# Performance work log

Measured on AMD Instinct MI355X. Metric: run time of the kernel, lower is better.

Reference implementation:

```python
import jax, jax.numpy as jnp
import numpy as np

START_IDX = 1  # undefined global `start_idx` in the source; fixed BOS id


def _lstm_gates(x_t, h, c, Wih, Whh, b):
    # PyTorch LSTM gate order: i, f, g, o
    gates = x_t @ Wih.T + h @ Whh.T + b
    i, f, g, o = jnp.split(gates, 4, axis=-1)
    c_new = jax.nn.sigmoid(f) * c + jax.nn.sigmoid(i) * jnp.tanh(g)
    h_new = jax.nn.sigmoid(o) * jnp.tanh(c_new)
    return h_new, c_new


def setup_inputs() -> dict:
    key = jax.random.key(0)
    ks = jax.random.split(key, 14)
    B, T, H, Vin, Vout = 64, 64, 512, 32000, 32000
    Hh = H // 2
    f = lambda k, shp, s=0.1: (jax.random.normal(k, shp) * s).astype(jnp.float32)
    return {
        "x": jax.random.randint(ks[0], (B, T), 0, Vin),
        "enc_emb": f(ks[1], (Vin, H), 0.2),
        "enc_wih_f": f(ks[2], (4 * Hh, H)),
        "enc_whh_f": f(ks[3], (4 * Hh, Hh)),
        "enc_b_f": jnp.zeros((4 * Hh,), jnp.float32),
        "enc_wih_b": f(ks[4], (4 * Hh, H)),
        "enc_whh_b": f(ks[5], (4 * Hh, Hh)),
        "enc_b_b": jnp.zeros((4 * Hh,), jnp.float32),
        "dec_emb": f(ks[6], (Vout, H), 0.2),
        "dec_wih": f(ks[7], (4 * H, H)),
        "dec_whh": f(ks[8], (4 * H, H)),
        "dec_b": jnp.zeros((4 * H,), jnp.float32),
        "clf_w": f(ks[9], (Vout, H), 0.2),
        "clf_b": jnp.zeros((Vout,), jnp.float32),
    }


def reference(x, enc_emb, enc_wih_f, enc_whh_f, enc_b_f,
              enc_wih_b, enc_whh_b, enc_b_b,
              dec_emb, dec_wih, dec_whh, dec_b, clf_w, clf_b):
    B, T = x.shape
    H = enc_emb.shape[1]
    Hh = H // 2

    # ---- Encoder: 1-layer bidirectional LSTM, hidden Hh per direction ----
    emb = enc_emb[x]                       # [B, T, H]
    xs = emb.transpose(1, 0, 2)            # [T, B, H] (scan over time)

    def run_dir(seq, Wih, Whh, b):
        def step(carry, xt):
            h, c = carry
            h, c = _lstm_gates(xt, h, c, Wih, Whh, b)
            return (h, c), None
        h0 = jnp.zeros((B, Hh), emb.dtype)
        (h, c), _ = jax.lax.scan(step, (h0, h0), seq)
        return h, c

    hf, cf = run_dir(xs, enc_wih_f, enc_whh_f, enc_b_f)
    hb, cb = run_dir(xs[::-1], enc_wih_b, enc_whh_b, enc_b_b)
    # hidden reshape in _forward_encoder: concat fwd/bwd final states -> [B, H]
    dec_h = jnp.concatenate([hf, hb], axis=-1)
    dec_c = jnp.concatenate([cf, cb], axis=-1)

    # ---- Decoder: greedy self-feeding loop for T-1 steps ----
    def dec_step(carry, _):
        h, c, y = carry
        e = dec_emb[y]                                  # [B, H]
        h, c = _lstm_gates(e, h, c, dec_wih, dec_whh, dec_b)
        logits = h @ clf_w.T + clf_b                    # [B, Vout]
        # argmax(softmax(logits)) == argmax(logits)
        y = jnp.argmax(logits, axis=-1)
        return (h, c, y), logits

    y0 = jnp.full((B,), START_IDX, dtype=x.dtype)
    _, logits = jax.lax.scan(dec_step, (dec_h, dec_c, y0), None, length=T - 1)
    # torch.cat(H, dim=2) with h.unsqueeze(2): [B, Vout, T-1]
    return logits.transpose(1, 2, 0)
```

## Files before the change

kernel.cpp:

```cpp
#include <hip/hip_runtime.h>
#include <math.h>

#define AM_PLAIN 0
#define AM_ENC   1
#define CM_PLAIN 0

typedef short bf16x8 __attribute__((ext_vector_type(8)));
typedef float f32x4 __attribute__((ext_vector_type(4)));

__device__ __forceinline__ float sigf(float x) { return 1.0f / (1.0f + expf(-x)); }

__device__ __forceinline__ unsigned short bf_rne(float f) {
  unsigned u = __float_as_uint(f);
  u += 0x7FFFu + ((u >> 16) & 1u);
  return (unsigned short)(u >> 16);
}
__device__ __forceinline__ float bf_f(unsigned short h) {
  return __uint_as_float(((unsigned)h) << 16);
}

template<int AMODE, int BTWO, int CMODE, int CDIR>
__global__ __launch_bounds__(256)
void gemm_k(const float* __restrict__ Ap, int lda,
            const float* __restrict__ emb,
            const int* __restrict__ xidx,
            const float* __restrict__ hbuf,
            const unsigned long long* __restrict__ cand_in, int nblk_cand, int step,
            const float* __restrict__ B0, const float* __restrict__ B1, int ldb,
            const float* __restrict__ bias,
            float* __restrict__ Cp, int ldc, long long zstride, int kper,
            unsigned long long* __restrict__ cand_out,
            float* __restrict__ dout, int tcol)
{
  __shared__ float As[32][68];
  __shared__ float Bs[32][68];
  __shared__ int ys[(AMODE == AM_PLAIN) ? 1 : 64];

  const int tid = threadIdx.x;
  const int tx = tid & 15, my = tid >> 4;
  const int n0 = tx * 4, m0 = my * 4;
  const int nbase = blockIdx.x * 64, mbase = blockIdx.y * 64;
  const int bz = blockIdx.z;

  if (AMODE == AM_ENC) {
    if (tid < 64) ys[tid] = xidx[tid * 64 + blockIdx.y];
  }
  if (AMODE != AM_PLAIN) __syncthreads();

  float acc[4][4];
#pragma unroll
  for (int i = 0; i < 4; ++i)
#pragma unroll
    for (int j = 0; j < 4; ++j) acc[i][j] = 0.0f;

  const int kbeg = bz * kper;
  const int lrow = tid >> 3, lk = (tid & 7) * 4;

  for (int kc = 0; kc < kper; kc += 32) {
    const int kg = kbeg + kc;
#pragma unroll
    for (int rr = 0; rr < 64; rr += 32) {
      const int row = lrow + rr;
      const float* ap;
      if (AMODE == AM_PLAIN) {
        ap = Ap + (size_t)(mbase + row) * lda + kg + lk;
      } else {
        ap = emb + (size_t)ys[row] * 512 + kg + lk;
      }
      const float4 v = *(const float4*)ap;
      As[lk + 0][row] = v.x; As[lk + 1][row] = v.y;
      As[lk + 2][row] = v.z; As[lk + 3][row] = v.w;

      const int n = nbase + row;
      const float* bp = B0 + (size_t)n * ldb + kg + lk;
      const float4 w = *(const float4*)bp;
      Bs[lk + 0][row] = w.x; Bs[lk + 1][row] = w.y;
      Bs[lk + 2][row] = w.z; Bs[lk + 3][row] = w.w;
    }
    __syncthreads();
#pragma unroll
    for (int k = 0; k < 32; ++k) {
      const float4 a = *(const float4*)&As[k][m0];
      const float4 b = *(const float4*)&Bs[k][n0];
      acc[0][0] += a.x * b.x; acc[0][1] += a.x * b.y; acc[0][2] += a.x * b.z; acc[0][3] += a.x * b.w;
      acc[1][0] += a.y * b.x; acc[1][1] += a.y * b.y; acc[1][2] += a.y * b.z; acc[1][3] += a.y * b.w;
      acc[2][0] += a.z * b.x; acc[2][1] += a.z * b.y; acc[2][2] += a.z * b.z; acc[2][3] += a.z * b.w;
      acc[3][0] += a.w * b.x; acc[3][1] += a.w * b.y; acc[3][2] += a.w * b.z; acc[3][3] += a.w * b.w;
    }
    __syncthreads();
  }

#pragma unroll
  for (int i = 0; i < 4; ++i) {
    const int m = mbase + m0 + i;
#pragma unroll
    for (int j = 0; j < 4; ++j) {
      const int n = nbase + n0 + j;
      float v = acc[i][j];
      if (bias) v += bias[n];
      Cp[bz * zstride + (size_t)m * ldc + n] = v;
    }
  }
}

__global__ __launch_bounds__(1024)
void enc_mstep(const float* __restrict__ xwf, const float* __restrict__ xwb,
               const short* __restrict__ whhfF, const short* __restrict__ whhfB,
               const short* __restrict__ hin, short* __restrict__ hout,
               float* __restrict__ cbuf, float* __restrict__ hfinal, int s)
{
  __shared__ float gl[2][4][64][16];

  const int blk = blockIdx.x;
  const int d = blk >> 4;
  const int jb = blk & 15;
  const int j0 = jb * 16;
  const float* xw = d ? xwb : xwf;
  const short* wf = d ? whhfB : whhfF;
  const short* hi_ = hin + d * 32768;
  short* ho_ = hout + d * 32768;
  const int t = d ? (63 - s) : s;

  const int tid = threadIdx.x;
  const int lane = tid & 63, wv = tid >> 6;
  const int g = wv & 3, mh = (wv >> 2) & 1, kh = wv >> 3;
  const int lrow = lane & 15, lq = lane >> 4;
  const int ntile = g * 16 + jb;

  f32x4 acc[2];
#pragma unroll
  for (int mtl = 0; mtl < 2; ++mtl) acc[mtl] = (f32x4){0.f, 0.f, 0.f, 0.f};

#pragma unroll
  for (int kk = 0; kk < 4; ++kk) {
    const int kc = kh * 4 + kk;
    const short* wb = wf + ((size_t)(ntile * 8 + kc)) * 1024 + lane * 8;
    const bf16x8 bhi = *(const bf16x8*)wb;
    const bf16x8 blo = *(const bf16x8*)(wb + 512);
#pragma unroll
    for (int mtl = 0; mtl < 2; ++mtl) {
      const int mt = mh * 2 + mtl;
      const short* ab = hi_ + ((size_t)(mt * 8 + kc)) * 1024 + lane * 8;
      const bf16x8 ahi = *(const bf16x8*)ab;
      const bf16x8 alo = *(const bf16x8*)(ab + 512);
      acc[mtl] = __builtin_amdgcn_mfma_f32_16x16x32_bf16(ahi, bhi, acc[mtl], 0, 0, 0);
      acc[mtl] = __builtin_amdgcn_mfma_f32_16x16x32_bf16(alo, bhi, acc[mtl], 0, 0, 0);
      acc[mtl] = __builtin_amdgcn_mfma_f32_16x16x32_bf16(ahi, blo, acc[mtl], 0, 0, 0);
    }
  }

#pragma unroll
  for (int mtl = 0; mtl < 2; ++mtl)
#pragma unroll
    for (int r = 0; r < 4; ++r) {
      const int b = (mh * 2 + mtl) * 16 + lq * 4 + r;
      gl[kh][g][b][lrow] = acc[mtl][r];
    }
  __syncthreads();

  {
    const int b = tid >> 4, jl = tid & 15;
    const int j = j0 + jl;
    const float* xrow = xw + ((size_t)(t * 64 + b)) * 1024;
    const float gi = gl[0][0][b][jl] + gl[1][0][b][jl] + xrow[0 * 256 + j];
    const float gf = gl[0][1][b][jl] + gl[1][1][b][jl] + xrow[1 * 256 + j];
    const float gg = gl[0][2][b][jl] + gl[1][2][b][jl] + xrow[2 * 256 + j];
    const float go = gl[0][3][b][jl] + gl[1][3][b][jl] + xrow[3 * 256 + j];
    const size_t off = (size_t)b * 512 + d * 256 + j;
    const float cn = sigf(gf) * cbuf[off] + sigf(gi) * tanhf(gg);
    cbuf[off] = cn;
    const float hn = sigf(go) * tanhf(cn);
    const unsigned short hh = bf_rne(hn);
    const unsigned short ll = bf_rne(hn - bf_f(hh));
    const int mt = b >> 4;
    const int base = ((mt * 8 + (j >> 5)) * 2) * 512 + (((j >> 3) & 3) * 16 + (b & 15)) * 8 + (j & 7);
    ho_[base] = (short)hh;
    ho_[base + 512] = (short)ll;
    if (s == 63) hfinal[off] = hn;
  }
}

__global__ void kinit2(float* __restrict__ c, int* __restrict__ he)
{
  const int i = blockIdx.x * 256 + threadIdx.x;
  if (i < 32768) { c[i] = 0.f; he[i] = 0; }
}

__global__ __launch_bounds__(256)
void wconv(const float* __restrict__ p0, const float* __restrict__ p1,
           int ld, int split, int KC, short* __restrict__ frag, int total)
{
  const int i = blockIdx.x * 256 + threadIdx.x;
  if (i >= total) return;
  const int lane = i & 63;
  const int ck = i >> 6;
  const int kc = ck % KC;
  const int nt = ck / KC;
  const int n = nt * 16 + (lane & 15);
  const int k0 = kc * 32 + (lane >> 4) * 8;
  const float* src = (k0 < split) ? (p0 + (size_t)n * ld + k0)
                                  : (p1 + (size_t)n * ld + (k0 - split));
  const float4 v0 = *(const float4*)src;
  const float4 v1 = *(const float4*)(src + 4);
  const float x[8] = {v0.x, v0.y, v0.z, v0.w, v1.x, v1.y, v1.z, v1.w};
  bf16x8 vh, vl;
#pragma unroll
  for (int e = 0; e < 8; ++e) {
    const unsigned short h = bf_rne(x[e]);
    vh[e] = (short)h;
    vl[e] = (short)bf_rne(x[e] - bf_f(h));
  }
  const size_t base = (size_t)ck * 1024 + lane * 8;
  *(bf16x8*)(frag + base) = vh;
  *(bf16x8*)(frag + base + 512) = vl;
}

__global__ __launch_bounds__(256)
void h2frag(const float* __restrict__ h, short* __restrict__ frag)
{
  const int i = blockIdx.x * 256 + threadIdx.x;
  const int lane = i & 63;
  const int ck = i >> 6;
  const int b = (ck >> 4) * 16 + (lane & 15);
  const int k0 = (ck & 15) * 32 + (lane >> 4) * 8;
  const float* src = h + (size_t)b * 512 + k0;
  const float4 v0 = *(const float4*)src;
  const float4 v1 = *(const float4*)(src + 4);
  const float x[8] = {v0.x, v0.y, v0.z, v0.w, v1.x, v1.y, v1.z, v1.w};
  bf16x8 vh, vl;
#pragma unroll
  for (int e = 0; e < 8; ++e) {
    const unsigned short hh = bf_rne(x[e]);
    vh[e] = (short)hh;
    vl[e] = (short)bf_rne(x[e] - bf_f(hh));
  }
  const size_t base = (size_t)ck * 1024 + lane * 8;
  *(bf16x8*)(frag + base) = vh;
  *(bf16x8*)(frag + base + 512) = vl;
}

__global__ __launch_bounds__(256)
void demb2bf(const float* __restrict__ demb, short* __restrict__ debf)
{
  const int i = blockIdx.x * 256 + threadIdx.x;
  if (i >= 2048000) return;
  const int r = i >> 6;
  const int k0 = (i & 63) * 8;
  const float* src = demb + (size_t)r * 512 + k0;
  const float4 v0 = *(const float4*)src;
  const float4 v1 = *(const float4*)(src + 4);
  const float x[8] = {v0.x, v0.y, v0.z, v0.w, v1.x, v1.y, v1.z, v1.w};
  bf16x8 vh, vl;
#pragma unroll
  for (int e = 0; e < 8; ++e) {
    const unsigned short h = bf_rne(x[e]);
    vh[e] = (short)h;
    vl[e] = (short)bf_rne(x[e] - bf_f(h));
  }
  *(bf16x8*)(debf + (size_t)r * 1024 + k0) = vh;
  *(bf16x8*)(debf + (size_t)r * 1024 + 512 + k0) = vl;
}

#define NBLK_CLF 500

__global__ __launch_bounds__(1024)
void dec_gates(const short* __restrict__ debf,
               const short* __restrict__ gfrag,
               const unsigned long long* __restrict__ cand, int step,
               const float* __restrict__ db,
               const short* __restrict__ hfin, short* __restrict__ hfout,
               float* __restrict__ cbuf)
{
  __shared__ int ys[64];
  __shared__ unsigned long long red[16 * 64];
  __shared__ float gl[2][4][64][16];

  const int tid = threadIdx.x;
  const int lane = tid & 63, wv = tid >> 6;
  const int g = wv & 3, mh = (wv >> 2) & 1, kh = wv >> 3;
  const int j0 = blockIdx.x * 16;
  const int ntile = g * 32 + blockIdx.x;
  const int lrow = lane & 15, lq = lane >> 4;

  if (step == 0) {
    if (tid < 64) ys[tid] = 1;
  } else {
    const int b = tid & 63, slot = tid >> 6;
    unsigned long long mv = 0;
    for (int i2 = slot; i2 < NBLK_CLF; i2 += 16) {
      const unsigned long long v = cand[(size_t)i2 * 64 + b];
      mv = v > mv ? v : mv;
    }
    red[slot * 64 + b] = mv;
    __syncthreads();
    if (tid < 64) {
      unsigned long long m = red[tid];
#pragma unroll
      for (int s2 = 1; s2 < 16; ++s2) {
        const unsigned long long v = red[s2 * 64 + tid];
        m = v > m ? v : m;
      }
      ys[tid] = (int)(0xFFFFFFFFu - (unsigned)(m & 0xFFFFFFFFull));
    }
  }
  __syncthreads();

  f32x4 acc[2];
#pragma unroll
  for (int mtl = 0; mtl < 2; ++mtl) acc[mtl] = (f32x4){0.f, 0.f, 0.f, 0.f};

  if (kh == 0) {
    for (int kc = 0; kc < 16; ++kc) {
      const short* wb = gfrag + ((size_t)(ntile * 32 + kc)) * 1024 + lane * 8;
      const bf16x8 bhi = *(const bf16x8*)wb;
      const bf16x8 blo = *(const bf16x8*)(wb + 512);
      const int k0 = kc * 32 + lq * 8;
#pragma unroll
      for (int mtl = 0; mtl < 2; ++mtl) {
        const int b = (mh * 2 + mtl) * 16 + lrow;
        const short* ap = debf + (size_t)ys[b] * 1024 + k0;
        const bf16x8 ahi = *(const bf16x8*)ap;
        const bf16x8 alo = *(const bf16x8*)(ap + 512);
        acc[mtl] = __builtin_amdgcn_mfma_f32_16x16x32_bf16(ahi, bhi, acc[mtl], 0, 0, 0);
        acc[mtl] = __builtin_amdgcn_mfma_f32_16x16x32_bf16(alo, bhi, acc[mtl], 0, 0, 0);
        acc[mtl] = __builtin_amdgcn_mfma_f32_16x16x32_bf16(ahi, blo, acc[mtl], 0, 0, 0);
      }
    }
  } else {
    for (int kc = 16; kc < 32; ++kc) {
      const short* wb = gfrag + ((size_t)(ntile * 32 + kc)) * 1024 + lane * 8;
      const bf16x8 bhi = *(const bf16x8*)wb;
      const bf16x8 blo = *(const bf16x8*)(wb + 512);
#pragma unroll
      for (int mtl = 0; mtl < 2; ++mtl) {
        const int mt = mh * 2 + mtl;
        const short* ab = hfin + ((size_t)(mt * 16 + (kc - 16))) * 1024 + lane * 8;
        const bf16x8 ahi = *(const bf16x8*)ab;
        const bf16x8 alo = *(const bf16x8*)(ab + 512);
        acc[mtl] = __builtin_amdgcn_mfma_f32_16x16x32_bf16(ahi, bhi, acc[mtl], 0, 0, 0);
        acc[mtl] = __builtin_amdgcn_mfma_f32_16x16x32_bf16(alo, bhi, acc[mtl], 0, 0, 0);
        acc[mtl] = __builtin_amdgcn_mfma_f32_16x16x32_bf16(ahi, blo, acc[mtl], 0, 0, 0);
      }
    }
  }

#pragma unroll
  for (int mtl = 0; mtl < 2; ++mtl)
#pragma unroll
    for (int r = 0; r < 4; ++r) {
      const int b = (mh * 2 + mtl) * 16 + lq * 4 + r;
      gl[kh][g][b][lrow] = acc[mtl][r];
    }
  __syncthreads();

  {
    const int b = tid >> 4, jl = tid & 15;
    const int j = j0 + jl;
    const float gi = gl[0][0][b][jl] + gl[1][0][b][jl] + db[j];
    const float gf = gl[0][1][b][jl] + gl[1][1][b][jl] + db[512 + j];
    const float gg = gl[0][2][b][jl] + gl[1][2][b][jl] + db[1024 + j];
    const float go = gl[0][3][b][jl] + gl[1][3][b][jl] + db[1536 + j];
    const size_t off = (size_t)b * 512 + j;
    const float cn = sigf(gf) * cbuf[off] + sigf(gi) * tanhf(gg);
    cbuf[off] = cn;
    const float hn = sigf(go) * tanhf(cn);
    const unsigned short hh = bf_rne(hn);
    const unsigned short hl2 = bf_rne(hn - bf_f(hh));
    const int mt = b >> 4;
    const int kc = j >> 5;
    const size_t base = ((size_t)(mt * 16 + kc)) * 1024 + ((((j & 31) >> 3) * 16) + (b & 15)) * 8 + (j & 7);
    hfout[base] = (short)hh;
    hfout[base + 512] = (short)hl2;
  }
}

template<int DIRECT>
__global__ __launch_bounds__(256)
void dec_clf(const short* __restrict__ hfrag, const short* __restrict__ wfrag,
             const float* __restrict__ clfb,
             float* __restrict__ dst, int tcol,
             unsigned long long* __restrict__ cand_out)
{
  __shared__ unsigned long long cl[4][64];
  const int tid = threadIdx.x;
  const int lane = tid & 63, wv = tid >> 6;
  const int ntile = blockIdx.x * 4 + wv;
  const int lrow = lane & 15, lq = lane >> 4;

  f32x4 acc[4];
#pragma unroll
  for (int mt = 0; mt < 4; ++mt) acc[mt] = (f32x4){0.f, 0.f, 0.f, 0.f};

#pragma unroll 2
  for (int kc = 0; kc < 16; ++kc) {
    const short* wb = wfrag + ((size_t)(ntile * 16 + kc)) * 1024 + lane * 8;
    const bf16x8 bhi = *(const bf16x8*)wb;
    const bf16x8 blo = *(const bf16x8*)(wb + 512);
#pragma unroll
    for (int mt = 0; mt < 4; ++mt) {
      const short* ab = hfrag + ((size_t)(mt * 16 + kc)) * 1024 + lane * 8;
      const bf16x8 ahi = *(const bf16x8*)ab;
      const bf16x8 alo = *(const bf16x8*)(ab + 512);
      acc[mt] = __builtin_amdgcn_mfma_f32_16x16x32_bf16(ahi, bhi, acc[mt], 0, 0, 0);
      acc[mt] = __builtin_amdgcn_mfma_f32_16x16x32_bf16(alo, bhi, acc[mt], 0, 0, 0);
      acc[mt] = __builtin_amdgcn_mfma_f32_16x16x32_bf16(ahi, blo, acc[mt], 0, 0, 0);
    }
  }

  const int v = ntile * 16 + lrow;
  const float bias = clfb[v];
#pragma unroll
  for (int mt = 0; mt < 4; ++mt) {
#pragma unroll
    for (int r = 0; r < 4; ++r) {
      const float val = acc[mt][r] + bias;
      const int b = mt * 16 + lq * 4 + r;
      if (DIRECT) __builtin_nontemporal_store(val, dst + ((size_t)b * 32000 + v) * 63 + tcol);
      else        __builtin_nontemporal_store(val, dst + (size_t)b * 32000 + v);
      unsigned u = __float_as_uint(val);
      u ^= (u & 0x80000000u) ? 0xFFFFFFFFu : 0x80000000u;
      unsigned long long p = ((unsigned long long)u << 32) |
                             (unsigned long long)(0xFFFFFFFFu - (unsigned)v);
#pragma unroll
      for (int m2 = 1; m2 < 16; m2 <<= 1) {
        const unsigned long long o = __shfl_xor(p, m2);
        p = o > p ? o : p;
      }
      if (lrow == 0) cl[wv][b] = p;
    }
  }
  __syncthreads();
  if (tid < 64) {
    unsigned long long m = cl[0][tid];
    const unsigned long long v1 = cl[1][tid];
    const unsigned long long v2 = cl[2][tid];
    const unsigned long long v3 = cl[3][tid];
    m = v1 > m ? v1 : m; m = v2 > m ? v2 : m; m = v3 > m ? v3 : m;
    cand_out[(size_t)blockIdx.x * 64 + tid] = m;
  }
}

__global__ __launch_bounds__(256)
void transpose_out(const float* __restrict__ ls, float* __restrict__ out)
{
  __shared__ float tile[128 * 63];
  const int b = blockIdx.y;
  const int v0 = blockIdx.x * 128;
  for (int idx = threadIdx.x; idx < 128 * 63; idx += 256) {
    const int t = idx >> 7, v = idx & 127;
    tile[v * 63 + t] = ls[((size_t)t * 64 + b) * 32000 + v0 + v];
  }
  __syncthreads();
  float4* o4 = (float4*)(out + ((size_t)b * 32000 + v0) * 63);
  const float4* t4 = (const float4*)tile;
  for (int i = threadIdx.x; i < (128 * 63) / 4; i += 256) o4[i] = t4[i];
}

extern "C" void kernel_launch(void* const* d_in, const int* in_sizes, int n_in,
                              void* d_out, int out_size, void* d_ws, size_t ws_size,
                              hipStream_t stream)
{
  const int*   x       = (const int*)d_in[0];
  const float* enc_emb = (const float*)d_in[1];
  const float* ewih_f  = (const float*)d_in[2];
  const float* ewhh_f  = (const float*)d_in[3];
  const float* eb_f    = (const float*)d_in[4];
  const float* ewih_b  = (const float*)d_in[5];
  const float* ewhh_b  = (const float*)d_in[6];
  const float* eb_b    = (const float*)d_in[7];
  const float* demb    = (const float*)d_in[8];
  const float* dwih    = (const float*)d_in[9];
  const float* dwhh    = (const float*)d_in[10];
  const float* db      = (const float*)d_in[11];
  const float* clfw    = (const float*)d_in[12];
  const float* clfb    = (const float*)d_in[13];
  float* out = (float*)d_out;
  float* ws  = (float*)d_ws;

  float* xwf = ws;
  float* xwb = xwf + 4194304;
  float* h0  = xwb + 4194304;
  float* h1  = h0 + 32768;
  float* cbf = h1 + 32768;
  unsigned long long* cand = (unsigned long long*)(cbf + 32768);
  short* wfrag  = (short*)(cbf + 32768 + 64000);
  short* gfrag  = wfrag + 32768000;
  short* hfragA = gfrag + 4194304;
  short* hfragB = hfragA + 65536;
  short* debf   = hfragB + 65536;
  short* ehfF   = debf + 32768000;
  short* ehfB   = ehfF + 524288;
  short* he0    = ehfB + 524288;
  short* he1    = he0 + 65536;
  float* ls = (float*)(he1 + 65536);
  const size_t need_f = 4194304ull * 2 + 32768ull * 3 + 64000ull
                      + 16384000ull + 2097152ull + 32768ull * 2
                      + 16384000ull + 262144ull * 2 + 32768ull * 2 + 129024000ull;
  const bool wspath = ws_size >= need_f * sizeof(float);

  kinit2<<<dim3(128), dim3(256), 0, stream>>>(cbf, (int*)he0);

  wconv<<<dim3(128), dim3(256), 0, stream>>>(ewhh_f, ewhh_f, 256, 256, 8, ehfF, 32768);
  wconv<<<dim3(128), dim3(256), 0, stream>>>(ewhh_b, ewhh_b, 256, 256, 8, ehfB, 32768);
  wconv<<<dim3(8000), dim3(256), 0, stream>>>(clfw, clfw, 512, 512, 16, wfrag, 2048000);
  wconv<<<dim3(1024), dim3(256), 0, stream>>>(dwih, dwhh, 512, 512, 32, gfrag, 262144);
  demb2bf<<<dim3(8000), dim3(256), 0, stream>>>(demb, debf);

  dim3 gx(16, 64, 1);
  gemm_k<AM_ENC, 0, CM_PLAIN, 0><<<gx, 256, 0, stream>>>(
      nullptr, 0, enc_emb, x, nullptr, nullptr, 0, 0,
      ewih_f, nullptr, 512, eb_f, xwf, 1024, 0, 512, nullptr, nullptr, 0);
  gemm_k<AM_ENC, 0, CM_PLAIN, 0><<<gx, 256, 0, stream>>>(
      nullptr, 0, enc_emb, x, nullptr, nullptr, 0, 0,
      ewih_b, nullptr, 512, eb_b, xwb, 1024, 0, 512, nullptr, nullptr, 0);

  for (int s = 0; s < 64; ++s) {
    const short* hin = (s & 1) ? he1 : he0;
    short* hout      = (s & 1) ? he0 : he1;
    enc_mstep<<<dim3(32), dim3(1024), 0, stream>>>(
        xwf, xwb, ehfF, ehfB, hin, hout, cbf, h0, s);
  }

  h2frag<<<dim3(16), dim3(256), 0, stream>>>(h0, hfragA);

  for (int t = 0; t < 63; ++t) {
    const short* hin = (t & 1) ? hfragB : hfragA;
    short* hout      = (t & 1) ? hfragA : hfragB;
    dec_gates<<<dim3(32), dim3(1024), 0, stream>>>(debf, gfrag, cand, t, db, hin, hout, cbf);
    if (wspath) {
      dec_clf<0><<<dim3(NBLK_CLF), dim3(256), 0, stream>>>(
          hout, wfrag, clfb, ls + (size_t)t * 2048000, t, cand);
    } else {
      dec_clf<1><<<dim3(NBLK_CLF), dim3(256), 0, stream>>>(
          hout, wfrag, clfb, out, t, cand);
    }
  }

  if (wspath) transpose_out<<<dim3(250, 64), 256, 0, stream>>>(ls, out);
}
```

Baseline: 3.922 ms.

## Prefetch classifier weight fragments via async global-to-LDS loads, three stages deep

The classifier kernel now streams its bf16 weight fragments through a 4-slot per-wave LDS ring buffer, filled by global_load_lds, keeping three k-chunks in flight ahead of the MFMA consumer. Explicit vmcnt waits and a sched_barrier order the loads against their use, and the k loop is fully unrolled with the A fragments loaded up front each iteration. The aim is to hide weight-streaming latency in a bandwidth-bound 32000-wide GEMV-like step repeated 63 times. It adds LDS usage and relies on exact vmcnt accounting, so a miscount would race with the hfrag register loads.

```diff
diff --git a/kernel.cpp b/kernel.cpp
--- a/kernel.cpp
+++ b/kernel.cpp
@@ -17,6 +17,12 @@
 }
 __device__ __forceinline__ float bf_f(unsigned short h) {
   return __uint_as_float(((unsigned)h) << 16);
+}
+
+__device__ __forceinline__ void gload16(const short* g, short* l) {
+  __builtin_amdgcn_global_load_lds(
+      (const __attribute__((address_space(1))) unsigned int*)g,
+      (__attribute__((address_space(3))) unsigned int*)l, 16, 0, 0);
 }
 
 template<int AMODE, int BTWO, int CMODE, int CDIR>
@@ -381,29 +387,48 @@
              float* __restrict__ dst, int tcol,
              unsigned long long* __restrict__ cand_out)
 {
+  __shared__ short wlds[4][4][1024];
   __shared__ unsigned long long cl[4][64];
   const int tid = threadIdx.x;
   const int lane = tid & 63, wv = tid >> 6;
   const int ntile = blockIdx.x * 4 + wv;
   const int lrow = lane & 15, lq = lane >> 4;
 
+#pragma unroll
+  for (int p = 0; p < 3; ++p) {
+    const short* src = wfrag + ((size_t)(ntile * 16 + p)) * 1024 + lane * 8;
+    gload16(src, &wlds[p][wv][0]);
+    gload16(src + 512, &wlds[p][wv][512]);
+  }
+
   f32x4 acc[4];
 #pragma unroll
   for (int mt = 0; mt < 4; ++mt) acc[mt] = (f32x4){0.f, 0.f, 0.f, 0.f};
 
-#pragma unroll 2
+#pragma unroll
   for (int kc = 0; kc < 16; ++kc) {
-    const short* wb = wfrag + ((size_t)(ntile * 16 + kc)) * 1024 + lane * 8;
-    const bf16x8 bhi = *(const bf16x8*)wb;
-    const bf16x8 blo = *(const bf16x8*)(wb + 512);
+    bf16x8 ah[4], al[4];
 #pragma unroll
     for (int mt = 0; mt < 4; ++mt) {
       const short* ab = hfrag + ((size_t)(mt * 16 + kc)) * 1024 + lane * 8;
-      const bf16x8 ahi = *(const bf16x8*)ab;
-      const bf16x8 alo = *(const bf16x8*)(ab + 512);
-      acc[mt] = __builtin_amdgcn_mfma_f32_16x16x32_bf16(ahi, bhi, acc[mt], 0, 0, 0);
-      acc[mt] = __builtin_amdgcn_mfma_f32_16x16x32_bf16(alo, bhi, acc[mt], 0, 0, 0);
-      acc[mt] = __builtin_amdgcn_mfma_f32_16x16x32_bf16(ahi, blo, acc[mt], 0, 0, 0);
+      ah[mt] = *(const bf16x8*)ab;
+      al[mt] = *(const bf16x8*)(ab + 512);
+    }
+    if (kc + 3 < 16) {
+      const short* src = wfrag + ((size_t)(ntile * 16 + kc + 3)) * 1024 + lane * 8;
+      gload16(src, &wlds[(kc + 3) & 3][wv][0]);
+      gload16(src + 512, &wlds[(kc + 3) & 3][wv][512]);
+    }
+    if (kc < 15) asm volatile("s_waitcnt vmcnt(6)" ::: "memory");
+    else         asm volatile("s_waitcnt vmcnt(0)" ::: "memory");
+    __builtin_amdgcn_sched_barrier(0);
+    const bf16x8 bhi = *(const bf16x8*)&wlds[kc & 3][wv][lane * 8];
+    const bf16x8 blo = *(const bf16x8*)&wlds[kc & 3][wv][512 + lane * 8];
+#pragma unroll
+    for (int mt = 0; mt < 4; ++mt) {
+      acc[mt] = __builtin_amdgcn_mfma_f32_16x16x32_bf16(ah[mt], bhi, acc[mt], 0, 0, 0);
+      acc[mt] = __builtin_amdgcn_mfma_f32_16x16x32_bf16(al[mt], bhi, acc[mt], 0, 0, 0);
+      acc[mt] = __builtin_amdgcn_mfma_f32_16x16x32_bf16(ah[mt], blo, acc[mt], 0, 0, 0);
     }
   }
 
```

New measurement: 3.990 ms. Within noise of the previous version (+1.7%).

## Compute encoder input projection with split-bf16 MFMA in one fused launch

Applied to the files above, without the earlier changes.

Replaces the fp32 SIMT tiled GEMM for the encoder input projection with a new kernel built on bf16 MFMA. Each operand is split into hi/lo bf16 parts and three MFMAs are accumulated to keep near-fp32 accuracy. Both directions are handled in one launch through blockIdx.z, and embedding rows are gathered straight from a pre-converted bf16 fragment table. In exchange, the full encoder embedding table and both input weight matrices are converted on every call. That adds memory traffic and workspace proportional to the vocabulary, even though only the gathered rows are used.

```diff
diff --git a/kernel.cpp b/kernel.cpp
--- a/kernel.cpp
+++ b/kernel.cpp
@@ -1,9 +1,5 @@
 #include <hip/hip_runtime.h>
 #include <math.h>
-
-#define AM_PLAIN 0
-#define AM_ENC   1
-#define CM_PLAIN 0
 
 typedef short bf16x8 __attribute__((ext_vector_type(8)));
 typedef float f32x4 __attribute__((ext_vector_type(4)));
@@ -19,88 +15,57 @@
   return __uint_as_float(((unsigned)h) << 16);
 }
 
-template<int AMODE, int BTWO, int CMODE, int CDIR>
 __global__ __launch_bounds__(256)
-void gemm_k(const float* __restrict__ Ap, int lda,
-            const float* __restrict__ emb,
-            const int* __restrict__ xidx,
-            const float* __restrict__ hbuf,
-            const unsigned long long* __restrict__ cand_in, int nblk_cand, int step,
-            const float* __restrict__ B0, const float* __restrict__ B1, int ldb,
-            const float* __restrict__ bias,
-            float* __restrict__ Cp, int ldc, long long zstride, int kper,
-            unsigned long long* __restrict__ cand_out,
-            float* __restrict__ dout, int tcol)
-{
-  __shared__ float As[32][68];
-  __shared__ float Bs[32][68];
-  __shared__ int ys[(AMODE == AM_PLAIN) ? 1 : 64];
-
+void enc_xproj(const short* __restrict__ eembf,
+               const int* __restrict__ x,
+               const short* __restrict__ ewfF, const short* __restrict__ ewfB,
+               const float* __restrict__ ebF, const float* __restrict__ ebB,
+               float* __restrict__ xwF, float* __restrict__ xwB)
+{
+  __shared__ int ys[64];
+  const int t = blockIdx.y, d = blockIdx.z;
+  const short* wf = d ? ewfB : ewfF;
+  const float* eb = d ? ebB : ebF;
+  float* xw = d ? xwB : xwF;
   const int tid = threadIdx.x;
-  const int tx = tid & 15, my = tid >> 4;
-  const int n0 = tx * 4, m0 = my * 4;
-  const int nbase = blockIdx.x * 64, mbase = blockIdx.y * 64;
-  const int bz = blockIdx.z;
-
-  if (AMODE == AM_ENC) {
-    if (tid < 64) ys[tid] = xidx[tid * 64 + blockIdx.y];
-  }
-  if (AMODE != AM_PLAIN) __syncthreads();
-
-  float acc[4][4];
-#pragma unroll
-  for (int i = 0; i < 4; ++i)
-#pragma unroll
-    for (int j = 0; j < 4; ++j) acc[i][j] = 0.0f;
-
-  const int kbeg = bz * kper;
-  const int lrow = tid >> 3, lk = (tid & 7) * 4;
-
-  for (int kc = 0; kc < kper; kc += 32) {
-    const int kg = kbeg + kc;
-#pragma unroll
-    for (int rr = 0; rr < 64; rr += 32) {
-      const int row = lrow + rr;
-      const float* ap;
-      if (AMODE == AM_PLAIN) {
-        ap = Ap + (size_t)(mbase + row) * lda + kg + lk;
-      } else {
-        ap = emb + (size_t)ys[row] * 512 + kg + lk;
-      }
-      const float4 v = *(const float4*)ap;
-      As[lk + 0][row] = v.x; As[lk + 1][row] = v.y;
-      As[lk + 2][row] = v.z; As[lk + 3][row] = v.w;
-
-      const int n = nbase + row;
-      const float* bp = B0 + (size_t)n * ldb + kg + lk;
-      const float4 w = *(const float4*)bp;
-      Bs[lk + 0][row] = w.x; Bs[lk + 1][row] = w.y;
-      Bs[lk + 2][row] = w.z; Bs[lk + 3][row] = w.w;
-    }
-    __syncthreads();
-#pragma unroll
-    for (int k = 0; k < 32; ++k) {
-      const float4 a = *(const float4*)&As[k][m0];
-      const float4 b = *(const float4*)&Bs[k][n0];
-      acc[0][0] += a.x * b.x; acc[0][1] += a.x * b.y; acc[0][2] += a.x * b.z; acc[0][3] += a.x * b.w;
-      acc[1][0] += a.y * b.x; acc[1][1] += a.y * b.y; acc[1][2] += a.y * b.z; acc[1][3] += a.y * b.w;
-      acc[2][0] += a.z * b.x; acc[2][1] += a.z * b.y; acc[2][2] += a.z * b.z; acc[2][3] += a.z * b.w;
-      acc[3][0] += a.w * b.x; acc[3][1] += a.w * b.y; acc[3][2] += a.w * b.z; acc[3][3] += a.w * b.w;
-    }
-    __syncthreads();
-  }
-
-#pragma unroll
-  for (int i = 0; i < 4; ++i) {
-    const int m = mbase + m0 + i;
-#pragma unroll
-    for (int j = 0; j < 4; ++j) {
-      const int n = nbase + n0 + j;
-      float v = acc[i][j];
-      if (bias) v += bias[n];
-      Cp[bz * zstride + (size_t)m * ldc + n] = v;
-    }
-  }
+  const int lane = tid & 63, wv = tid >> 6;
+  const int ntile = blockIdx.x * 4 + wv;
+  const int lrow = lane & 15, lq = lane >> 4;
+
+  if (tid < 64) ys[tid] = x[tid * 64 + t];
+  __syncthreads();
+
+  f32x4 acc[4];
+#pragma unroll
+  for (int mt = 0; mt < 4; ++mt) acc[mt] = (f32x4){0.f, 0.f, 0.f, 0.f};
+
+#pragma unroll 2
+  for (int kc = 0; kc < 16; ++kc) {
+    const short* wb = wf + ((size_t)(ntile * 16 + kc)) * 1024 + lane * 8;
+    const bf16x8 bhi = *(const bf16x8*)wb;
+    const bf16x8 blo = *(const bf16x8*)(wb + 512);
+    const int k0 = kc * 32 + lq * 8;
+#pragma unroll
+    for (int mt = 0; mt < 4; ++mt) {
+      const int b = mt * 16 + lrow;
+      const short* ap = eembf + (size_t)ys[b] * 1024 + k0;
+      const bf16x8 ahi = *(const bf16x8*)ap;
+      const bf16x8 alo = *(const bf16x8*)(ap + 512);
+      acc[mt] = __builtin_amdgcn_mfma_f32_16x16x32_bf16(ahi, bhi, acc[mt], 0, 0, 0);
+      acc[mt] = __builtin_amdgcn_mfma_f32_16x16x32_bf16(alo, bhi, acc[mt], 0, 0, 0);
+      acc[mt] = __builtin_amdgcn_mfma_f32_16x16x32_bf16(ahi, blo, acc[mt], 0, 0, 0);
+    }
+  }
+
+  const int n = ntile * 16 + lrow;
+  const float bias = eb[n];
+#pragma unroll
+  for (int mt = 0; mt < 4; ++mt)
+#pragma unroll
+    for (int r = 0; r < 4; ++r) {
+      const int b = mt * 16 + lq * 4 + r;
+      xw[((size_t)(t * 64 + b)) * 1024 + n] = acc[mt][r] + bias;
+    }
 }
 
 __global__ __launch_bounds__(1024)
@@ -492,27 +457,29 @@
   short* ehfB   = ehfF + 524288;
   short* he0    = ehfB + 524288;
   short* he1    = he0 + 65536;
-  float* ls = (float*)(he1 + 65536);
+  short* eembf  = he1 + 65536;
+  short* ewfF   = eembf + 32768000;
+  short* ewfB   = ewfF + 1048576;
+  float* ls = (float*)(ewfB + 1048576);
   const size_t need_f = 4194304ull * 2 + 32768ull * 3 + 64000ull
                       + 16384000ull + 2097152ull + 32768ull * 2
-                      + 16384000ull + 262144ull * 2 + 32768ull * 2 + 129024000ull;
+                      + 16384000ull + 262144ull * 2 + 32768ull * 2
+                      + 16384000ull + 524288ull * 2 + 129024000ull;
   const bool wspath = ws_size >= need_f * sizeof(float);
 
   kinit2<<<dim3(128), dim3(256), 0, stream>>>(cbf, (int*)he0);
 
   wconv<<<dim3(128), dim3(256), 0, stream>>>(ewhh_f, ewhh_f, 256, 256, 8, ehfF, 32768);
   wconv<<<dim3(128), dim3(256), 0, stream>>>(ewhh_b, ewhh_b, 256, 256, 8, ehfB, 32768);
+  wconv<<<dim3(256), dim3(256), 0, stream>>>(ewih_f, ewih_f, 512, 512, 16, ewfF, 65536);
+  wconv<<<dim3(256), dim3(256), 0, stream>>>(ewih_b, ewih_b, 512, 512, 16, ewfB, 65536);
   wconv<<<dim3(8000), dim3(256), 0, stream>>>(clfw, clfw, 512, 512, 16, wfrag, 2048000);
   wconv<<<dim3(1024), dim3(256), 0, stream>>>(dwih, dwhh, 512, 512, 32, gfrag, 262144);
   demb2bf<<<dim3(8000), dim3(256), 0, stream>>>(demb, debf);
-
-  dim3 gx(16, 64, 1);
-  gemm_k<AM_ENC, 0, CM_PLAIN, 0><<<gx, 256, 0, stream>>>(
-      nullptr, 0, enc_emb, x, nullptr, nullptr, 0, 0,
-      ewih_f, nullptr, 512, eb_f, xwf, 1024, 0, 512, nullptr, nullptr, 0);
-  gemm_k<AM_ENC, 0, CM_PLAIN, 0><<<gx, 256, 0, stream>>>(
-      nullptr, 0, enc_emb, x, nullptr, nullptr, 0, 0,
-      ewih_b, nullptr, 512, eb_b, xwb, 1024, 0, 512, nullptr, nullptr, 0);
+  demb2bf<<<dim3(8000), dim3(256), 0, stream>>>(enc_emb, eembf);
+
+  enc_xproj<<<dim3(16, 64, 2), dim3(256), 0, stream>>>(
+      eembf, x, ewfF, ewfB, eb_f, eb_b, xwf, xwb);
 
   for (int s = 0; s < 64; ++s) {
     const short* hin = (s & 1) ? he1 : he0;
```

Measured after the change: 3.971 ms, median of 2. No clear change (+1.2%).
